# Optimization experiments

Measured on AMD Instinct MI355X. Metric: run time of the kernel, lower is better.

## Reference

```python
import jax, jax.numpy as jnp
import numpy as np

N_NODES = 100000
N_EDGES = 400000
N_GRAPHS = 2000
IN_DIM = 58
HEADS = 4
HID = 64           # per-head hidden = output_dim // heads = 256 // 4
OUT = 256
NEG_SLOPE = 0.2    # PyG GATConv default


def _glorot(key, shape):
    fan_in, fan_out = shape[0], shape[-1]
    lim = jnp.sqrt(6.0 / (fan_in + fan_out)).astype(jnp.float32)
    return jax.random.uniform(key, shape, jnp.float32, -lim, lim)


def setup_inputs() -> dict:
    key = jax.random.key(0)
    ks = jax.random.split(key, 16)
    x = jax.random.normal(ks[0], (N_NODES, IN_DIM), jnp.float32)
    edge_index = jax.random.randint(ks[1], (2, N_EDGES), 0, N_NODES, jnp.int64)
    batch = jnp.sort(jax.random.randint(ks[2], (N_NODES,), 0, N_GRAPHS, jnp.int64))
    return {
        "x": x,
        "edge_index": edge_index,
        "batch": batch,
        # layer 1: 58 -> 4 heads x 64, concat -> 256
        "W1": _glorot(ks[3], (IN_DIM, HEADS * HID)),
        "a_src1": _glorot(ks[4], (HEADS, HID)),
        "a_dst1": _glorot(ks[5], (HEADS, HID)),
        "b1": jnp.zeros((HEADS * HID,), jnp.float32),
        # layer 2: 256 -> 4 heads x 64, concat -> 256
        "W2": _glorot(ks[6], (HEADS * HID, HEADS * HID)),
        "a_src2": _glorot(ks[7], (HEADS, HID)),
        "a_dst2": _glorot(ks[8], (HEADS, HID)),
        "b2": jnp.zeros((HEADS * HID,), jnp.float32),
        # layer 3: 256 -> 1 head x 256, no concat (mean over 1 head)
        "W3": _glorot(ks[9], (HEADS * HID, OUT)),
        "a_src3": _glorot(ks[10], (1, OUT)),
        "a_dst3": _glorot(ks[11], (1, OUT)),
        "b3": jnp.zeros((OUT,), jnp.float32),
    }


def _gat_layer(x, src, dst, W, a_src, a_dst, b, heads, ch, concat):
    n = x.shape[0]
    h = (x @ W).reshape(n, heads, ch)                      # [N,H,C]
    e_src = jnp.einsum("nhc,hc->nh", h, a_src)             # [N,H]
    e_dst = jnp.einsum("nhc,hc->nh", h, a_dst)
    e = jax.nn.leaky_relu(e_src[src] + e_dst[dst], NEG_SLOPE)  # [E,H]
    # segment softmax over destination nodes (self-loops ensure non-empty segments)
    m = jax.ops.segment_max(e, dst, num_segments=n)
    ex = jnp.exp(e - m[dst])
    denom = jax.ops.segment_sum(ex, dst, num_segments=n)
    coef = ex / denom[dst]                                 # [E,H]
    out = jax.ops.segment_sum(h[src] * coef[:, :, None], dst, num_segments=n)
    out = out.reshape(n, heads * ch) if concat else out.mean(axis=1)
    return out + b


def reference(x, edge_index, batch, W1, a_src1, a_dst1, b1,
              W2, a_src2, a_dst2, b2, W3, a_src3, a_dst3, b3):
    n = x.shape[0]
    loops = jnp.arange(n, dtype=edge_index.dtype)
    src = jnp.concatenate([edge_index[0], loops])          # add_self_loops (PyG default)
    dst = jnp.concatenate([edge_index[1], loops])
    h = jax.nn.relu(_gat_layer(x, src, dst, W1, a_src1, a_dst1, b1, HEADS, HID, True))
    h = jax.nn.relu(_gat_layer(h, src, dst, W2, a_src2, a_dst2, b2, HEADS, HID, True))
    h = _gat_layer(h, src, dst, W3, a_src3, a_dst3, b3, 1, OUT, False)
    # global max pool over graphs
    return jax.ops.segment_max(h, batch, num_segments=N_GRAPHS)
```

## Files before the change

### kernel.cpp

```cpp
#include <hip/hip_runtime.h>
#include <hip/hip_bf16.h>
#include <math.h>

#define N_NODES_C 100000
#define E_ORIG    400000
#define E_TOT     500000
#define E_PAD     (E_TOT + 3 * N_NODES_C)
#define N_GRAPHS_C 2000
#define KDIM      256

typedef __attribute__((ext_vector_type(8))) short short8v;
typedef __attribute__((ext_vector_type(4))) float f32x4;

__device__ __forceinline__ void gload_lds16(const void* g, void* l) {
    __builtin_amdgcn_global_load_lds(
        (const __attribute__((address_space(1))) unsigned int*)g,
        (__attribute__((address_space(3))) unsigned int*)l, 16, 0, 0);
}

__device__ __forceinline__ float bflo(unsigned u) { return __uint_as_float(u << 16); }
__device__ __forceinline__ float bfhi(unsigned u) { return __uint_as_float(u & 0xffff0000u); }

#define XE  (N_NODES_C * 64)
#define W1E (256 * 64)
#define WBE (256 * 256)
__global__ __launch_bounds__(256) void conv_all_count(
        const float* __restrict__ x, const float* __restrict__ W1,
        const float* __restrict__ W2, const float* __restrict__ W3,
        const int* __restrict__ ei,
        __hip_bfloat16* __restrict__ Xb, __hip_bfloat16* __restrict__ Wt1,
        __hip_bfloat16* __restrict__ Wt2, __hip_bfloat16* __restrict__ Wt3,
        int* __restrict__ deg) {
    int idx = blockIdx.x * 256 + threadIdx.x;
    if (idx < E_TOT) {
        int d = (idx < E_ORIG) ? ei[E_ORIG + idx] : (idx - E_ORIG);
        atomicAdd(&deg[d], 1);
    }
    if (idx < XE) {
        int row = idx >> 6, c = idx & 63;
        float v = (c < 58) ? x[row * 58 + c] : 0.f;
        Xb[idx] = __float2bfloat16(v);
    } else if (idx < XE + W1E) {
        int i = idx - XE;
        int c = i >> 6, k = i & 63;
        float v = (k < 58) ? W1[k * 256 + c] : 0.f;
        Wt1[i] = __float2bfloat16(v);
    } else if (idx < XE + W1E + WBE) {
        int i = idx - XE - W1E;
        int c = i >> 8, k = i & 255;
        Wt2[i] = __float2bfloat16(W2[k * 256 + c]);
    } else if (idx < XE + W1E + 2 * WBE) {
        int i = idx - XE - W1E - WBE;
        int c = i >> 8, k = i & 255;
        Wt3[i] = __float2bfloat16(W3[k * 256 + c]);
    }
}

__global__ void scan_chunk(const int* __restrict__ in, int* __restrict__ out,
                           int* __restrict__ partials, int n) {
    __shared__ int s[256];
    int tid = threadIdx.x;
    int i = blockIdx.x * 256 + tid;
    int dv = (i < n) ? in[i] : 0;
    int v = (dv + 3) & ~3;
    s[tid] = v;
    __syncthreads();
    for (int off = 1; off < 256; off <<= 1) {
        int t = (tid >= off) ? s[tid - off] : 0;
        __syncthreads();
        s[tid] += t;
        __syncthreads();
    }
    if (i < n) out[i] = s[tid] - v;
    if (tid == 255) partials[blockIdx.x] = s[255];
}

__global__ void scan_fix(int* __restrict__ rowoff, const int* __restrict__ partials, int n) {
    __shared__ int sred[256];
    int t = threadIdx.x;
    int acc = 0;
    for (int i = t; i < blockIdx.x; i += 256) acc += partials[i];
    sred[t] = acc;
    __syncthreads();
    for (int off = 128; off; off >>= 1) {
        if (t < off) sred[t] += sred[t + off];
        __syncthreads();
    }
    int base = sred[0];
    int i = blockIdx.x * 256 + t;
    if (i < n) rowoff[i] += base;
}

__global__ void scatter_k(const int* __restrict__ ei, const int* __restrict__ rowoff,
                          int* cursor, int* __restrict__ csr_src,
                          int* __restrict__ csr_dst, const int* __restrict__ deg) {
    int e = blockIdx.x * 256 + threadIdx.x;
    if (e < E_TOT) {
        int s, d;
        if (e < E_ORIG) { s = ei[e]; d = ei[E_ORIG + e]; }
        else            { s = e - E_ORIG; d = s; }
        int pos = rowoff[d] + atomicAdd(&cursor[d], 1);
        csr_src[pos] = s;
        csr_dst[pos] = d;
    }
    if (e < N_NODES_C) {
        int dg = deg[e];
        int pd = (dg + 3) & ~3;
        int base = rowoff[e];
        for (int j = dg; j < pd; j++) {
            csr_src[base + j] = e | 0x80000000;
            csr_dst[base + j] = e;
        }
    }
}

template <int KPAD, int NH>
__global__ __launch_bounds__(256, 2) void gemm_mfma(
        const __hip_bfloat16* __restrict__ Xb, const __hip_bfloat16* __restrict__ Wt,
        const float* __restrict__ ASRC, const float* __restrict__ ADST,
        __hip_bfloat16* __restrict__ H, float* __restrict__ ES, float* __restrict__ ED) {
    __shared__ char As[128 * 128];
    __shared__ char Bs[256 * 128];
    __shared__ float red[2][128][2];

    const int t = threadIdx.x;
    const int wv = t >> 6, lane = t & 63;
    const int wr = wv >> 1, wc = wv & 1;
    const int r15 = lane & 15, hi = lane >> 4;
    const int n0 = blockIdx.x * 128;
    const int srow = lane >> 3;
    const int sx = ((lane & 7) ^ srow) * 16;
    constexpr int KB = KPAD * 2;

    f32x4 acc[4][8];
#pragma unroll
    for (int m = 0; m < 4; m++)
#pragma unroll
        for (int n = 0; n < 8; n++) acc[m][n] = (f32x4){0.f, 0.f, 0.f, 0.f};

    for (int kt = 0; kt < KPAD / 64; kt++) {
        if (kt) __syncthreads();
        const int k0b = kt * 128;
#pragma unroll
        for (int p = 0; p < 4; p++) {
            int i = wv * 4 + p;
            int gr = n0 + i * 8 + srow;
            if (gr > N_NODES_C - 1) gr = N_NODES_C - 1;
            gload_lds16((const char*)Xb + (size_t)gr * KB + k0b + sx, As + i * 1024);
        }
#pragma unroll
        for (int p = 0; p < 8; p++) {
            int i = wv * 8 + p;
            int col = i * 8 + srow;
            gload_lds16((const char*)Wt + (size_t)col * KB + k0b + sx, Bs + i * 1024);
        }
        asm volatile("s_waitcnt vmcnt(0)" ::: "memory");
        __syncthreads();

#pragma unroll
        for (int ks = 0; ks < 2; ks++) {
            const int cx = ((ks * 4 + hi) ^ (r15 & 7)) * 16;
            short8v a[4];
#pragma unroll
            for (int m = 0; m < 4; m++)
                a[m] = *(const short8v*)(As + (wr * 64 + m * 16 + r15) * 128 + cx);
#pragma unroll
            for (int n = 0; n < 8; n++) {
                short8v b = *(const short8v*)(Bs + (wc * 128 + n * 16 + r15) * 128 + cx);
#pragma unroll
                for (int m = 0; m < 4; m++)
                    acc[m][n] = __builtin_amdgcn_mfma_f32_16x16x32_bf16(a[m], b, acc[m][n], 0, 0, 0);
            }
        }
    }

    float asv[8], adv[8];
#pragma unroll
    for (int n = 0; n < 8; n++) {
        int col = wc * 128 + n * 16 + r15;
        asv[n] = ASRC[col];
        adv[n] = ADST[col];
    }

#pragma unroll
    for (int m = 0; m < 4; m++) {
#pragma unroll
        for (int j = 0; j < 4; j++) {
            int lrow = wr * 64 + m * 16 + hi * 4 + j;
            int row = n0 + lrow;
            bool ok = row < N_NODES_C;
            if (ok) {
#pragma unroll
                for (int n = 0; n < 8; n++)
                    H[(size_t)row * KDIM + wc * 128 + n * 16 + r15] =
                        __float2bfloat16(acc[m][n][j]);
            }
            if (NH == 4) {
                float p0s = 0.f, p1s = 0.f, p0d = 0.f, p1d = 0.f;
#pragma unroll
                for (int n = 0; n < 4; n++) {
                    p0s = fmaf(acc[m][n][j], asv[n], p0s);
                    p0d = fmaf(acc[m][n][j], adv[n], p0d);
                    p1s = fmaf(acc[m][n + 4][j], asv[n + 4], p1s);
                    p1d = fmaf(acc[m][n + 4][j], adv[n + 4], p1d);
                }
#pragma unroll
                for (int s = 8; s; s >>= 1) {
                    p0s += __shfl_xor(p0s, s, 16);
                    p0d += __shfl_xor(p0d, s, 16);
                    p1s += __shfl_xor(p1s, s, 16);
                    p1d += __shfl_xor(p1d, s, 16);
                }
                if (r15 == 0 && ok) {
                    ES[row * 4 + wc * 2 + 0] = p0s;
                    ES[row * 4 + wc * 2 + 1] = p1s;
                    ED[row * 4 + wc * 2 + 0] = p0d;
                    ED[row * 4 + wc * 2 + 1] = p1d;
                }
            } else {
                float ps = 0.f, pd = 0.f;
#pragma unroll
                for (int n = 0; n < 8; n++) {
                    ps = fmaf(acc[m][n][j], asv[n], ps);
                    pd = fmaf(acc[m][n][j], adv[n], pd);
                }
#pragma unroll
                for (int s = 8; s; s >>= 1) {
                    ps += __shfl_xor(ps, s, 16);
                    pd += __shfl_xor(pd, s, 16);
                }
                if (r15 == 0) { red[0][lrow][wc] = ps; red[1][lrow][wc] = pd; }
            }
        }
    }
    if (NH == 1) {
        __syncthreads();
        if (t < 128) {
            int row = n0 + t;
            if (row < N_NODES_C) {
                ES[row] = red[0][t][0] + red[0][t][1];
                ED[row] = red[1][t][0] + red[1][t][1];
            }
        }
    }
}

#define ECAP 160
template <int NH, bool RELU>
__global__ __launch_bounds__(256) void agg_kernel(
        const __hip_bfloat16* __restrict__ H, const int* __restrict__ rowoff,
        const int* __restrict__ csr_src, const int* __restrict__ csr_dst,
        const float* __restrict__ ES, const float* __restrict__ ED,
        const float* __restrict__ bias, __hip_bfloat16* __restrict__ Out) {
    __shared__ float Els[ECAP * NH];
    __shared__ int   Sls[ECAP];
    __shared__ int   roff[9];
    int t = threadIdx.x;
    int n0 = blockIdx.x * 8;
    if (t < 9) roff[t] = rowoff[n0 + t];
    __syncthreads();
    int beg0 = roff[0];
    int ne = roff[8] - beg0;
    int nl = (ne < ECAP) ? ne : ECAP;
    for (int j = t; j < nl; j += 256) {
        int slot = beg0 + j;
        int srcj = csr_src[slot];
        bool padj = srcj < 0;
        srcj &= 0x7fffffff;
        int dj = csr_dst[slot];
        Sls[j] = srcj;
        if (NH == 4) {
            float4 es = *(const float4*)&ES[srcj * 4];
            float4 ed = *(const float4*)&ED[dj * 4];
            float e;
            e = es.x + ed.x; e = (e > 0.f) ? e : 0.2f * e; Els[j * 4 + 0] = padj ? -1e30f : e;
            e = es.y + ed.y; e = (e > 0.f) ? e : 0.2f * e; Els[j * 4 + 1] = padj ? -1e30f : e;
            e = es.z + ed.z; e = (e > 0.f) ? e : 0.2f * e; Els[j * 4 + 2] = padj ? -1e30f : e;
            e = es.w + ed.w; e = (e > 0.f) ? e : 0.2f * e; Els[j * 4 + 3] = padj ? -1e30f : e;
        } else {
            float e = ES[srcj] + ED[dj];
            e = (e > 0.f) ? e : 0.2f * e;
            Els[j] = padj ? -1e30f : e;
        }
    }
    __syncthreads();

    int g = t >> 5;
    int node = n0 + g;
    int l = t & 31;
    int c0 = l * 8;
    int head = (NH == 4) ? (l >> 3) : 0;
    int jb = roff[g] - beg0, je = roff[g + 1] - beg0;
    int jeF = (je < ECAP) ? je : ECAP;

    float m = -1e30f;
    for (int j = jb; j < jeF; j++) m = fmaxf(m, Els[j * NH + head]);
    if (je > ECAP) {
        float edv = ED[node * NH + head];
        for (int j = ECAP; j < je; j++) {
            int sj = csr_src[beg0 + j];
            if (sj < 0) continue;
            float e = ES[sj * NH + head] + edv;
            e = (e > 0.f) ? e : 0.2f * e;
            m = fmaxf(m, e);
        }
    }

    float s = 0.f;
    float a[8];
#pragma unroll
    for (int i = 0; i < 8; i++) a[i] = 0.f;
    const unsigned short* Hu = (const unsigned short*)H;

#define ACC8(v, p) \
    a[0] = fmaf(p, bflo(v.x), a[0]); a[1] = fmaf(p, bfhi(v.x), a[1]); \
    a[2] = fmaf(p, bflo(v.y), a[2]); a[3] = fmaf(p, bfhi(v.y), a[3]); \
    a[4] = fmaf(p, bflo(v.z), a[4]); a[5] = fmaf(p, bfhi(v.z), a[5]); \
    a[6] = fmaf(p, bflo(v.w), a[6]); a[7] = fmaf(p, bfhi(v.w), a[7]);

    int j = jb;
    for (; j + 4 <= jeF; j += 4) {
        int s0 = Sls[j], s1 = Sls[j + 1], s2 = Sls[j + 2], s3 = Sls[j + 3];
        float e0 = Els[(j + 0) * NH + head], e1 = Els[(j + 1) * NH + head];
        float e2 = Els[(j + 2) * NH + head], e3 = Els[(j + 3) * NH + head];
        uint4 v0 = *(const uint4*)(Hu + (size_t)s0 * KDIM + c0);
        uint4 v1 = *(const uint4*)(Hu + (size_t)s1 * KDIM + c0);
        uint4 v2 = *(const uint4*)(Hu + (size_t)s2 * KDIM + c0);
        uint4 v3 = *(const uint4*)(Hu + (size_t)s3 * KDIM + c0);
        float p0 = __expf(e0 - m), p1 = __expf(e1 - m);
        float p2 = __expf(e2 - m), p3 = __expf(e3 - m);
        s += p0 + p1 + p2 + p3;
        ACC8(v0, p0)
        ACC8(v1, p1)
        ACC8(v2, p2)
        ACC8(v3, p3)
    }
    for (; j < jeF; j++) {
        int s0 = Sls[j];
        float e0 = Els[j * NH + head];
        uint4 v0 = *(const uint4*)(Hu + (size_t)s0 * KDIM + c0);
        float p0 = __expf(e0 - m);
        s += p0;
        ACC8(v0, p0)
    }
    if (je > ECAP) {
        float edv = ED[node * NH + head];
        for (int jj = ECAP; jj < je; jj++) {
            int sj = csr_src[beg0 + jj];
            if (sj < 0) continue;
            float e = ES[sj * NH + head] + edv;
            e = (e > 0.f) ? e : 0.2f * e;
            float p = __expf(e - m);
            s += p;
            uint4 v = *(const uint4*)(Hu + (size_t)sj * KDIM + c0);
            ACC8(v, p)
        }
    }
#undef ACC8

    float inv = 1.f / s;
    float4 b0 = *(const float4*)&bias[c0];
    float4 b1 = *(const float4*)&bias[c0 + 4];
    float o[8];
    o[0] = fmaf(a[0], inv, b0.x); o[1] = fmaf(a[1], inv, b0.y);
    o[2] = fmaf(a[2], inv, b0.z); o[3] = fmaf(a[3], inv, b0.w);
    o[4] = fmaf(a[4], inv, b1.x); o[5] = fmaf(a[5], inv, b1.y);
    o[6] = fmaf(a[6], inv, b1.z); o[7] = fmaf(a[7], inv, b1.w);
    __hip_bfloat16 rb[8];
#pragma unroll
    for (int i = 0; i < 8; i++) {
        float v = RELU ? fmaxf(o[i], 0.f) : o[i];
        rb[i] = __float2bfloat16(v);
    }
    *(uint4*)&Out[(size_t)node * KDIM + c0] = *(uint4*)rb;
}

__global__ __launch_bounds__(256) void pool_k(
        const __hip_bfloat16* __restrict__ O, const int* __restrict__ batch,
        float* __restrict__ out) {
    __shared__ int range[2];
    __shared__ float red[3][256];
    int g = blockIdx.x, k = threadIdx.x;
    if (k < 2) {
        int v = g + k;
        int lo = 0, hi = N_NODES_C;
        while (lo < hi) { int mid = (lo + hi) >> 1; if (batch[mid] < v) lo = mid + 1; else hi = mid; }
        range[k] = lo;
    }
    __syncthreads();
    int cg = k & 63;
    int ro = k >> 6;
    float m0 = -INFINITY, m1 = -INFINITY, m2 = -INFINITY, m3 = -INFINITY;
    const unsigned short* Ou = (const unsigned short*)O;
    for (int i = range[0] + ro; i < range[1]; i += 4) {
        uint2 v = *(const uint2*)(Ou + (size_t)i * KDIM + cg * 4);
        m0 = fmaxf(m0, bflo(v.x)); m1 = fmaxf(m1, bfhi(v.x));
        m2 = fmaxf(m2, bflo(v.y)); m3 = fmaxf(m3, bfhi(v.y));
    }
    if (ro) {
        red[ro - 1][cg * 4 + 0] = m0; red[ro - 1][cg * 4 + 1] = m1;
        red[ro - 1][cg * 4 + 2] = m2; red[ro - 1][cg * 4 + 3] = m3;
    }
    __syncthreads();
    if (ro == 0) {
        m0 = fmaxf(fmaxf(m0, red[0][cg * 4 + 0]), fmaxf(red[1][cg * 4 + 0], red[2][cg * 4 + 0]));
        m1 = fmaxf(fmaxf(m1, red[0][cg * 4 + 1]), fmaxf(red[1][cg * 4 + 1], red[2][cg * 4 + 1]));
        m2 = fmaxf(fmaxf(m2, red[0][cg * 4 + 2]), fmaxf(red[1][cg * 4 + 2], red[2][cg * 4 + 2]));
        m3 = fmaxf(fmaxf(m3, red[0][cg * 4 + 3]), fmaxf(red[1][cg * 4 + 3], red[2][cg * 4 + 3]));
        float4 o = make_float4(m0, m1, m2, m3);
        *(float4*)&out[(size_t)g * KDIM + cg * 4] = o;
    }
}

extern "C" void kernel_launch(void* const* d_in, const int* in_sizes, int n_in,
                              void* d_out, int out_size, void* d_ws, size_t ws_size,
                              hipStream_t stream) {
    const float* x     = (const float*)d_in[0];
    const int*   ei    = (const int*)d_in[1];
    const int*   batch = (const int*)d_in[2];
    const float* W1  = (const float*)d_in[3];
    const float* as1 = (const float*)d_in[4];
    const float* ad1 = (const float*)d_in[5];
    const float* b1  = (const float*)d_in[6];
    const float* W2  = (const float*)d_in[7];
    const float* as2 = (const float*)d_in[8];
    const float* ad2 = (const float*)d_in[9];
    const float* b2  = (const float*)d_in[10];
    const float* W3  = (const float*)d_in[11];
    const float* as3 = (const float*)d_in[12];
    const float* ad3 = (const float*)d_in[13];
    const float* b3  = (const float*)d_in[14];
    float* out = (float*)d_out;

    char* p = (char*)d_ws;
    auto alloc = [&](size_t bytes) { char* r = p; p += (bytes + 255) & ~(size_t)255; return r; };
    __hip_bfloat16* Xb  = (__hip_bfloat16*)alloc((size_t)N_NODES_C * 64 * 2);
    __hip_bfloat16* Hb  = (__hip_bfloat16*)alloc((size_t)N_NODES_C * KDIM * 2);
    __hip_bfloat16* Nb  = (__hip_bfloat16*)alloc((size_t)N_NODES_C * KDIM * 2);
    __hip_bfloat16* Wt1 = (__hip_bfloat16*)alloc(256 * 64 * 2);
    __hip_bfloat16* Wt2 = (__hip_bfloat16*)alloc(256 * 256 * 2);
    __hip_bfloat16* Wt3 = (__hip_bfloat16*)alloc(256 * 256 * 2);
    float* ES     = (float*)alloc((size_t)N_NODES_C * 4 * 4);
    float* ED     = (float*)alloc((size_t)N_NODES_C * 4 * 4);
    int* degcur   = (int*)alloc((size_t)(2 * N_NODES_C + 1) * 4);
    int* deg      = degcur;
    int* cursor   = degcur + (N_NODES_C + 1);
    int* rowoff   = (int*)alloc((N_NODES_C + 1) * 4);
    int* csr      = (int*)alloc((size_t)E_PAD * 4 + 256);
    int* csrd     = (int*)alloc((size_t)E_PAD * 4);
    int* partials = (int*)alloc(512 * 4);

    hipMemsetAsync(degcur, 0, (size_t)(2 * N_NODES_C + 1) * 4, stream);
    int ctot = XE + W1E + 2 * WBE;
    conv_all_count<<<(ctot + 255) / 256, 256, 0, stream>>>(
        x, W1, W2, W3, ei, Xb, Wt1, Wt2, Wt3, deg);

    int nb = (N_NODES_C + 1 + 255) / 256;
    scan_chunk<<<nb, 256, 0, stream>>>(deg, rowoff, partials, N_NODES_C + 1);
    scan_fix<<<nb, 256, 0, stream>>>(rowoff, partials, N_NODES_C + 1);
    int egrid = (E_TOT + 255) / 256;
    scatter_k<<<egrid, 256, 0, stream>>>(ei, rowoff, cursor, csr, csrd, deg);

    int ggrid = (N_NODES_C + 127) / 128;
    int agrid = N_NODES_C / 8;
    gemm_mfma<64, 4><<<ggrid, 256, 0, stream>>>(Xb, Wt1, as1, ad1, Hb, ES, ED);
    agg_kernel<4, true><<<agrid, 256, 0, stream>>>(Hb, rowoff, csr, csrd, ES, ED, b1, Nb);
    gemm_mfma<256, 4><<<ggrid, 256, 0, stream>>>(Nb, Wt2, as2, ad2, Hb, ES, ED);
    agg_kernel<4, true><<<agrid, 256, 0, stream>>>(Hb, rowoff, csr, csrd, ES, ED, b2, Nb);
    gemm_mfma<256, 1><<<ggrid, 256, 0, stream>>>(Nb, Wt3, as3, ad3, Hb, ES, ED);
    agg_kernel<1, false><<<agrid, 256, 0, stream>>>(Hb, rowoff, csr, csrd, ES, ED, b3, Nb);
    pool_k<<<N_GRAPHS_C, 256, 0, stream>>>(Nb, batch, out);
}
```

Before: 315.6 us.

## Fuse global max pool into final aggregation and use 8-wave GEMM blocks

The final aggregation kernel now writes its outputs straight into the pooled result with order-preserving unsigned atomicMax, replacing the separate pool kernel and the write and re-read of the layer-3 node features. A small decode kernel turns the encoded values back into floats, mapping untouched (zero) slots to -inf. Separately, the GEMM moves from 256 to 512 threads per block, so each wave computes half as many rows with fewer accumulators, which lowers register pressure and may raise occupancy. The fusion adds contended atomics on the per-graph rows, and the fused path skips the bf16 rounding that the old pool applied to its input, so results may differ slightly.

```diff
diff --git a/kernel.cpp b/kernel.cpp
--- a/kernel.cpp
+++ b/kernel.cpp
@@ -115,7 +115,7 @@
 }
 
 template <int KPAD, int NH>
-__global__ __launch_bounds__(256, 2) void gemm_mfma(
+__global__ __launch_bounds__(512, 4) void gemm_mfma(
         const __hip_bfloat16* __restrict__ Xb, const __hip_bfloat16* __restrict__ Wt,
         const float* __restrict__ ASRC, const float* __restrict__ ADST,
         __hip_bfloat16* __restrict__ H, float* __restrict__ ES, float* __restrict__ ED) {
@@ -132,9 +132,9 @@
     const int sx = ((lane & 7) ^ srow) * 16;
     constexpr int KB = KPAD * 2;
 
-    f32x4 acc[4][8];
-#pragma unroll
-    for (int m = 0; m < 4; m++)
+    f32x4 acc[2][8];
+#pragma unroll
+    for (int m = 0; m < 2; m++)
 #pragma unroll
         for (int n = 0; n < 8; n++) acc[m][n] = (f32x4){0.f, 0.f, 0.f, 0.f};
 
@@ -142,15 +142,15 @@
         if (kt) __syncthreads();
         const int k0b = kt * 128;
 #pragma unroll
-        for (int p = 0; p < 4; p++) {
-            int i = wv * 4 + p;
+        for (int p = 0; p < 2; p++) {
+            int i = wv * 2 + p;
             int gr = n0 + i * 8 + srow;
             if (gr > N_NODES_C - 1) gr = N_NODES_C - 1;
             gload_lds16((const char*)Xb + (size_t)gr * KB + k0b + sx, As + i * 1024);
         }
 #pragma unroll
-        for (int p = 0; p < 8; p++) {
-            int i = wv * 8 + p;
+        for (int p = 0; p < 4; p++) {
+            int i = wv * 4 + p;
             int col = i * 8 + srow;
             gload_lds16((const char*)Wt + (size_t)col * KB + k0b + sx, Bs + i * 1024);
         }
@@ -160,16 +160,13 @@
 #pragma unroll
         for (int ks = 0; ks < 2; ks++) {
             const int cx = ((ks * 4 + hi) ^ (r15 & 7)) * 16;
-            short8v a[4];
-#pragma unroll
-            for (int m = 0; m < 4; m++)
-                a[m] = *(const short8v*)(As + (wr * 64 + m * 16 + r15) * 128 + cx);
+            short8v a0 = *(const short8v*)(As + (wr * 32 + 0  + r15) * 128 + cx);
+            short8v a1 = *(const short8v*)(As + (wr * 32 + 16 + r15) * 128 + cx);
 #pragma unroll
             for (int n = 0; n < 8; n++) {
                 short8v b = *(const short8v*)(Bs + (wc * 128 + n * 16 + r15) * 128 + cx);
-#pragma unroll
-                for (int m = 0; m < 4; m++)
-                    acc[m][n] = __builtin_amdgcn_mfma_f32_16x16x32_bf16(a[m], b, acc[m][n], 0, 0, 0);
+                acc[0][n] = __builtin_amdgcn_mfma_f32_16x16x32_bf16(a0, b, acc[0][n], 0, 0, 0);
+                acc[1][n] = __builtin_amdgcn_mfma_f32_16x16x32_bf16(a1, b, acc[1][n], 0, 0, 0);
             }
         }
     }
@@ -183,10 +180,10 @@
     }
 
 #pragma unroll
-    for (int m = 0; m < 4; m++) {
+    for (int m = 0; m < 2; m++) {
 #pragma unroll
         for (int j = 0; j < 4; j++) {
-            int lrow = wr * 64 + m * 16 + hi * 4 + j;
+            int lrow = wr * 32 + m * 16 + hi * 4 + j;
             int row = n0 + lrow;
             bool ok = row < N_NODES_C;
             if (ok) {
@@ -246,12 +243,13 @@
 }
 
 #define ECAP 160
-template <int NH, bool RELU>
+template <int NH, bool RELU, bool POOL>
 __global__ __launch_bounds__(256) void agg_kernel(
         const __hip_bfloat16* __restrict__ H, const int* __restrict__ rowoff,
         const int* __restrict__ csr_src, const int* __restrict__ csr_dst,
         const float* __restrict__ ES, const float* __restrict__ ED,
-        const float* __restrict__ bias, __hip_bfloat16* __restrict__ Out) {
+        const float* __restrict__ bias, __hip_bfloat16* __restrict__ Out,
+        const int* __restrict__ batch, unsigned* __restrict__ outw) {
     __shared__ float Els[ECAP * NH];
     __shared__ int   Sls[ECAP];
     __shared__ int   roff[9];
@@ -366,50 +364,33 @@
     o[2] = fmaf(a[2], inv, b0.z); o[3] = fmaf(a[3], inv, b0.w);
     o[4] = fmaf(a[4], inv, b1.x); o[5] = fmaf(a[5], inv, b1.y);
     o[6] = fmaf(a[6], inv, b1.z); o[7] = fmaf(a[7], inv, b1.w);
-    __hip_bfloat16 rb[8];
-#pragma unroll
-    for (int i = 0; i < 8; i++) {
-        float v = RELU ? fmaxf(o[i], 0.f) : o[i];
-        rb[i] = __float2bfloat16(v);
-    }
-    *(uint4*)&Out[(size_t)node * KDIM + c0] = *(uint4*)rb;
-}
-
-__global__ __launch_bounds__(256) void pool_k(
-        const __hip_bfloat16* __restrict__ O, const int* __restrict__ batch,
-        float* __restrict__ out) {
-    __shared__ int range[2];
-    __shared__ float red[3][256];
-    int g = blockIdx.x, k = threadIdx.x;
-    if (k < 2) {
-        int v = g + k;
-        int lo = 0, hi = N_NODES_C;
-        while (lo < hi) { int mid = (lo + hi) >> 1; if (batch[mid] < v) lo = mid + 1; else hi = mid; }
-        range[k] = lo;
-    }
-    __syncthreads();
-    int cg = k & 63;
-    int ro = k >> 6;
-    float m0 = -INFINITY, m1 = -INFINITY, m2 = -INFINITY, m3 = -INFINITY;
-    const unsigned short* Ou = (const unsigned short*)O;
-    for (int i = range[0] + ro; i < range[1]; i += 4) {
-        uint2 v = *(const uint2*)(Ou + (size_t)i * KDIM + cg * 4);
-        m0 = fmaxf(m0, bflo(v.x)); m1 = fmaxf(m1, bfhi(v.x));
-        m2 = fmaxf(m2, bflo(v.y)); m3 = fmaxf(m3, bfhi(v.y));
-    }
-    if (ro) {
-        red[ro - 1][cg * 4 + 0] = m0; red[ro - 1][cg * 4 + 1] = m1;
-        red[ro - 1][cg * 4 + 2] = m2; red[ro - 1][cg * 4 + 3] = m3;
-    }
-    __syncthreads();
-    if (ro == 0) {
-        m0 = fmaxf(fmaxf(m0, red[0][cg * 4 + 0]), fmaxf(red[1][cg * 4 + 0], red[2][cg * 4 + 0]));
-        m1 = fmaxf(fmaxf(m1, red[0][cg * 4 + 1]), fmaxf(red[1][cg * 4 + 1], red[2][cg * 4 + 1]));
-        m2 = fmaxf(fmaxf(m2, red[0][cg * 4 + 2]), fmaxf(red[1][cg * 4 + 2], red[2][cg * 4 + 2]));
-        m3 = fmaxf(fmaxf(m3, red[0][cg * 4 + 3]), fmaxf(red[1][cg * 4 + 3], red[2][cg * 4 + 3]));
-        float4 o = make_float4(m0, m1, m2, m3);
-        *(float4*)&out[(size_t)g * KDIM + cg * 4] = o;
-    }
+    if (POOL) {
+        int gr = batch[node];
+        unsigned* base = outw + (size_t)gr * KDIM + c0;
+#pragma unroll
+        for (int i = 0; i < 8; i++) {
+            int bi = __float_as_int(o[i]);
+            unsigned enc = (bi >= 0) ? ((unsigned)bi | 0x80000000u) : ~(unsigned)bi;
+            atomicMax(&base[i], enc);
+        }
+    } else {
+        __hip_bfloat16 rb[8];
+#pragma unroll
+        for (int i = 0; i < 8; i++) {
+            float v = RELU ? fmaxf(o[i], 0.f) : o[i];
+            rb[i] = __float2bfloat16(v);
+        }
+        *(uint4*)&Out[(size_t)node * KDIM + c0] = *(uint4*)rb;
+    }
+}
+
+__global__ __launch_bounds__(256) void decode_k(unsigned* __restrict__ w, int n) {
+    int i = blockIdx.x * 256 + threadIdx.x;
+    if (i >= n) return;
+    unsigned u = w[i];
+    unsigned b = (u & 0x80000000u) ? (u & 0x7fffffffu) : ~u;
+    if (u == 0u) b = 0xFF800000u;
+    w[i] = b;
 }
 
 extern "C" void kernel_launch(void* const* d_in, const int* in_sizes, int n_in,
@@ -430,7 +411,7 @@
     const float* as3 = (const float*)d_in[12];
     const float* ad3 = (const float*)d_in[13];
     const float* b3  = (const float*)d_in[14];
-    float* out = (float*)d_out;
+    unsigned* outw = (unsigned*)d_out;
 
     char* p = (char*)d_ws;
     auto alloc = [&](size_t bytes) { char* r = p; p += (bytes + 255) & ~(size_t)255; return r; };
@@ -451,6 +432,7 @@
     int* partials = (int*)alloc(512 * 4);
 
     hipMemsetAsync(degcur, 0, (size_t)(2 * N_NODES_C + 1) * 4, stream);
+    hipMemsetAsync(outw, 0, (size_t)out_size * 4, stream);
     int ctot = XE + W1E + 2 * WBE;
     conv_all_count<<<(ctot + 255) / 256, 256, 0, stream>>>(
         x, W1, W2, W3, ei, Xb, Wt1, Wt2, Wt3, deg);
@@ -463,11 +445,11 @@
 
     int ggrid = (N_NODES_C + 127) / 128;
     int agrid = N_NODES_C / 8;
-    gemm_mfma<64, 4><<<ggrid, 256, 0, stream>>>(Xb, Wt1, as1, ad1, Hb, ES, ED);
-    agg_kernel<4, true><<<agrid, 256, 0, stream>>>(Hb, rowoff, csr, csrd, ES, ED, b1, Nb);
-    gemm_mfma<256, 4><<<ggrid, 256, 0, stream>>>(Nb, Wt2, as2, ad2, Hb, ES, ED);
-    agg_kernel<4, true><<<agrid, 256, 0, stream>>>(Hb, rowoff, csr, csrd, ES, ED, b2, Nb);
-    gemm_mfma<256, 1><<<ggrid, 256, 0, stream>>>(Nb, Wt3, as3, ad3, Hb, ES, ED);
-    agg_kernel<1, false><<<agrid, 256, 0, stream>>>(Hb, rowoff, csr, csrd, ES, ED, b3, Nb);
-    pool_k<<<N_GRAPHS_C, 256, 0, stream>>>(Nb, batch, out);
-}
+    gemm_mfma<64, 4><<<ggrid, 512, 0, stream>>>(Xb, Wt1, as1, ad1, Hb, ES, ED);
+    agg_kernel<4, true, false><<<agrid, 256, 0, stream>>>(Hb, rowoff, csr, csrd, ES, ED, b1, Nb, batch, outw);
+    gemm_mfma<256, 4><<<ggrid, 512, 0, stream>>>(Nb, Wt2, as2, ad2, Hb, ES, ED);
+    agg_kernel<4, true, false><<<agrid, 256, 0, stream>>>(Hb, rowoff, csr, csrd, ES, ED, b2, Nb, batch, outw);
+    gemm_mfma<256, 1><<<ggrid, 512, 0, stream>>>(Nb, Wt3, as3, ad3, Hb, ES, ED);
+    agg_kernel<1, false, true><<<agrid, 256, 0, stream>>>(Hb, rowoff, csr, csrd, ES, ED, b3, Nb, batch, outw);
+    decode_k<<<(out_size + 255) / 256, 256, 0, stream>>>(outw, out_size);
+}
```

Result: slower. 864.4 us (+173.9%).
